# Performance work log

Hardware: AMD Instinct MI355X
Metric: run time of the kernel (lower is better)

Reference implementation:

```python
import jax, jax.numpy as jnp
import numpy as np

THRESHOLD = 0.05
STRIDE = (1, 1)
PADDING = ((1, 1), (1, 1))


def ternary_quantize(w, threshold=THRESHOLD):
    # w -> {-1, 0, +1}; zero where |w| <= threshold
    mask = (jnp.abs(w) > threshold).astype(w.dtype)
    return jnp.sign(w) * mask


def setup_inputs() -> dict:
    key = jax.random.key(0)
    k1, k2 = jax.random.split(key)
    B, Cin, H, W = 32, 256, 56, 56
    Cout, kH, kW = 256, 3, 3
    fan_in = Cin * kH * kW
    std = np.sqrt(2.0 / fan_in) * 2.0
    x = jax.random.normal(k1, (B, Cin, H, W), dtype=jnp.float32)
    weight = jax.random.normal(k2, (Cout, Cin, kH, kW), dtype=jnp.float32) * std
    bias = jnp.zeros((Cout,), dtype=jnp.float32)
    return {"x": x, "weight": weight, "bias": bias}


def reference(x, weight, bias):
    w_t = ternary_quantize(weight, THRESHOLD)
    out = jax.lax.conv_general_dilated(
        x, w_t,
        window_strides=STRIDE,
        padding=PADDING,
        dimension_numbers=("NCHW", "OIHW", "NCHW"),
    )
    return out + bias[None, :, None, None]
```

## Files before the change

### kernel.cpp

```cpp
#include <hip/hip_runtime.h>

#define CIN   256
#define COUT  256
#define HH    56
#define WW    56
#define BATCH 32
#define KTOT  2304
#define HP    58
#define WP    58
#define NPIX  (BATCH*HH*WW)
#define HWSZ  (HH*WW)
#define BN    224
#define NBLK  (NPIX/BN)

typedef __bf16 bf16x8 __attribute__((ext_vector_type(8)));
typedef float  f32x4  __attribute__((ext_vector_type(4)));

#define AS1 __attribute__((address_space(1)))
#define AS3 __attribute__((address_space(3)))

__device__ __forceinline__ unsigned short f2bf(float f) {
  union { float f; unsigned int u; } v; v.f = f;
  unsigned int u = v.u;
  u += 0x7fffu + ((u >> 16) & 1u);
  return (unsigned short)(u >> 16);
}

__device__ __forceinline__ void async16(const void* g, void* l) {
  __builtin_amdgcn_global_load_lds((const AS1 unsigned int*)g,
                                   (AS3 unsigned int*)l, 16, 0, 0);
}

#define TSTR 60
#define QBLKS 2304
__global__ __launch_bounds__(256) void prep(const float* __restrict__ w,
                                            unsigned short* __restrict__ wr,
                                            const float* __restrict__ x,
                                            unsigned short* __restrict__ xp) {
  const int bx = blockIdx.x;
  if (bx < QBLKS) {
    int tid = bx * 256 + threadIdx.x;
    int co  = tid / KTOT;
    int rem = tid - co * KTOT;
    int tap = rem >> 8;
    int ci  = rem & 255;
    int kh  = tap / 3;
    int kw  = tap - kh * 3;
    float v = w[((co * CIN + ci) * 3 + kh) * 3 + kw];
    float q = (fabsf(v) > 0.05f) ? ((v > 0.f) ? 1.f : -1.f) : 0.f;
    wr[tid] = f2bf(q);
    return;
  }
  const int pbx = bx - QBLKS;
  const int nhp = pbx >> 2;
  const int n   = nhp / HP;
  const int hp  = nhp - n * HP;
  const int ci0 = (pbx & 3) << 6;
  const int t   = threadIdx.x;
  const size_t obase = (size_t)nhp * (WP * 256);

  __shared__ __align__(16) float tile[64 * TSTR];
  const bool hborder = (hp == 0) || (hp == HP - 1);

  if (!hborder) {
    const int h = hp - 1;
    #pragma unroll
    for (int it = 0; it < 4; ++it) {
      int linear = it * 256 + t;
      if (linear < 896) {
        int cil = linear / 14;
        int w4  = linear - cil * 14;
        *(float4*)&tile[cil * TSTR + w4 * 4] =
            *(const float4*)&x[(((size_t)(n * CIN + ci0 + cil)) * HH + h) * WW + w4 * 4];
      }
    }
  }
  __syncthreads();

  #pragma unroll
  for (int it = 0; it < 2; ++it) {
    int linear = it * 256 + t;
    if (linear < 464) {
      int wp = linear >> 3;
      int g  = linear & 7;
      unsigned int pk[4] = {0u, 0u, 0u, 0u};
      if (!hborder && wp != 0 && wp != WP - 1) {
        #pragma unroll
        for (int j = 0; j < 4; ++j) {
          int jr = (j + g) & 3;
          unsigned int lo = f2bf(tile[(g * 8 + 2 * jr) * TSTR + (wp - 1)]);
          unsigned int hi = f2bf(tile[(g * 8 + 2 * jr + 1) * TSTR + (wp - 1)]);
          pk[jr] = lo | (hi << 16);
        }
      }
      uint4 v; v.x = pk[0]; v.y = pk[1]; v.z = pk[2]; v.w = pk[3];
      *(uint4*)(xp + obase + (size_t)wp * 256 + ci0 + g * 8) = v;
    }
  }
}


#define NOWAIT (void)0
#define VM4 asm volatile("s_waitcnt vmcnt(4)" ::: "memory")
#define VM0 asm volatile("s_waitcnt vmcnt(0)" ::: "memory")

#define STAGE4(buf_, kn_) do {                                                \
  const int kn__ = (kn_);                                                     \
  const size_t koW_ = (size_t)kn__ << 5;                                      \
  const int tap_ = kn__ >> 3;                                                 \
  const int kh_  = tap_ / 3;                                                  \
  const int kw_  = tap_ - kh_ * 3;                                            \
  const size_t koX_ = (size_t)((kh_ * WP + kw_) * 256 + ((kn__ & 7) << 5));   \
  char* da_ = smem + (buf_) * 32768 + t * 16;                                 \
  char* db_ = smem + (buf_) * 32768 + 16384 + t * 16;                         \
  async16(Wr + koW_ + aSrc0, da_);                                            \
  async16(Wr + koW_ + aSrc1, da_ + 8192);                                     \
  async16(Xp + koX_ + bSrc0, db_);                                            \
  async16(Xp + koX_ + bSrc1, db_ + 8192);                                     \
} while (0)

#define PHASE(buf_, WAITE, ...) do {                                          \
  __VA_ARGS__;                                                                \
  bf16x8 af_[4], bf_[7];                                                      \
  _Pragma("unroll")                                                           \
  for (int mt = 0; mt < 4; ++mt)                                              \
    af_[mt] = *(const bf16x8*)(smem + (buf_) * 32768 + rdA + mt * 1024);      \
  _Pragma("unroll")                                                           \
  for (int nt = 0; nt < 7; ++nt)                                              \
    bf_[nt] = *(const bf16x8*)(smem + (buf_) * 32768 + 16384 + rdB + nt * 1024);\
  _Pragma("unroll")                                                           \
  for (int mt = 0; mt < 4; ++mt)                                              \
    _Pragma("unroll")                                                         \
    for (int nt = 0; nt < 7; ++nt)                                            \
      acc[mt][nt] = __builtin_amdgcn_mfma_f32_16x16x32_bf16(                  \
          af_[mt], bf_[nt], acc[mt][nt], 0, 0, 0);                            \
  WAITE;                                                                      \
  __builtin_amdgcn_s_barrier();                                               \
  __builtin_amdgcn_sched_barrier(0);                                          \
} while (0)

__global__ __launch_bounds__(512, 2) void conv_gemm(
    const unsigned short* __restrict__ Wr,
    const unsigned short* __restrict__ Xp,
    const float* __restrict__ bias,
    float* __restrict__ out) {
  extern __shared__ char smem[];

  const int t    = threadIdx.x;
  const int lane = t & 63;
  const int wv   = t >> 6;
  const int wm   = wv >> 1;
  const int wn   = wv & 1;
  const int l15  = lane & 15;
  const int quad = lane >> 4;

  const int bid = blockIdx.x;
  const int pb  = (bid & 7) * 56 + (bid >> 3);
  const int p0  = pb * BN;

  const int srow = t >> 2;
  const int schk = (t & 3) ^ ((srow >> 1) & 3);

  const size_t aSrc0 = (size_t)srow * KTOT + schk * 8;
  const size_t aSrc1 = aSrc0 + (size_t)128 * KTOT;

  const int pA = p0 + srow;
  const int pB = pA + 128;
  const int nA = pA / HWSZ;  const int hwA = pA - nA * HWSZ;
  const int hA = hwA / WW;   const int wA  = hwA - hA * WW;
  const int nB = pB / HWSZ;  const int hwB = pB - nB * HWSZ;
  const int hB = hwB / WW;   const int wB  = hwB - hB * WW;
  const size_t bSrc0 = ((size_t)((nA * HP + hA) * WP + wA)) * 256 + schk * 8;
  const size_t bSrc1 = ((size_t)((nB * HP + hB) * WP + wB)) * 256 + schk * 8;

  const int rchk = (quad ^ ((l15 >> 1) & 3)) * 16;
  const int rdA  = (wm * 64  + l15) * 64 + rchk;
  const int rdB  = (wn * 112 + l15) * 64 + rchk;

  f32x4 acc[4][7];
  #pragma unroll
  for (int i = 0; i < 4; ++i)
    #pragma unroll
    for (int j = 0; j < 7; ++j)
      acc[i][j] = (f32x4){0.f, 0.f, 0.f, 0.f};

  STAGE4(0, 0);
  STAGE4(1, 1);
  VM4;
  __builtin_amdgcn_s_barrier();
  __builtin_amdgcn_sched_barrier(0);

  #pragma unroll 1
  for (int it = 0; it < 23; ++it) {
    const int k0 = 3 * it;
    PHASE(0, VM4, STAGE4(2, k0 + 2));
    PHASE(1, VM4, STAGE4(0, k0 + 3));
    PHASE(2, VM4, STAGE4(1, k0 + 4));
  }
  PHASE(0, VM4, STAGE4(2, 71));
  PHASE(1, VM0, NOWAIT);
  PHASE(2, NOWAIT, NOWAIT);

  float bv[4][4];
  #pragma unroll
  for (int mt = 0; mt < 4; ++mt)
    #pragma unroll
    for (int r = 0; r < 4; ++r)
      bv[mt][r] = bias[wm * 64 + mt * 16 + quad * 4 + r];

  #pragma unroll
  for (int nt = 0; nt < 7; ++nt) {
    const int p  = p0 + wn * 112 + nt * 16 + l15;
    const int np = p / HWSZ;
    const int hw = p - np * HWSZ;
    const size_t obase = (size_t)np * (COUT * HWSZ) + hw;
    #pragma unroll
    for (int mt = 0; mt < 4; ++mt) {
      const int co = wm * 64 + mt * 16 + quad * 4;
      #pragma unroll
      for (int r = 0; r < 4; ++r)
        out[obase + (size_t)(co + r) * HWSZ] = acc[mt][nt][r] + bv[mt][r];
    }
  }
}

extern "C" void kernel_launch(void* const* d_in, const int* in_sizes, int n_in,
                              void* d_out, int out_size, void* d_ws, size_t ws_size,
                              hipStream_t stream) {
  const float* x    = (const float*)d_in[0];
  const float* w    = (const float*)d_in[1];
  const float* bias = (const float*)d_in[2];
  float* out        = (float*)d_out;

  unsigned short* xp = (unsigned short*)d_ws;
  unsigned short* wr = (unsigned short*)((char*)d_ws + 55115776);

  prep<<<dim3(QBLKS + BATCH * HP * 4), dim3(256), 0, stream>>>(w, wr, x, xp);

  (void)hipFuncSetAttribute((const void*)conv_gemm,
                            hipFuncAttributeMaxDynamicSharedMemorySize, 98304);
  conv_gemm<<<dim3(NBLK), dim3(512), 98304, stream>>>(wr, xp, bias, out);
}
```

Measured before the change: 308.0 us.

## Deepen LDS pipeline to four stages and double-buffer B fragments in registers

```diff
diff --git a/kernel.cpp b/kernel.cpp
--- a/kernel.cpp
+++ b/kernel.cpp
@@ -119,21 +119,23 @@
   async16(Xp + koX_ + bSrc1, db_ + 8192);                                     \
 } while (0)
 
-#define PHASE(buf_, WAITE, ...) do {                                          \
+#define PHASE(bc_, bn_, cur_, nxt_, DOBF_, WAITE, ...) do {                   \
   __VA_ARGS__;                                                                \
-  bf16x8 af_[4], bf_[7];                                                      \
+  bf16x8 af_[4];                                                              \
   _Pragma("unroll")                                                           \
   for (int mt = 0; mt < 4; ++mt)                                              \
-    af_[mt] = *(const bf16x8*)(smem + (buf_) * 32768 + rdA + mt * 1024);      \
-  _Pragma("unroll")                                                           \
-  for (int nt = 0; nt < 7; ++nt)                                              \
-    bf_[nt] = *(const bf16x8*)(smem + (buf_) * 32768 + 16384 + rdB + nt * 1024);\
+    af_[mt] = *(const bf16x8*)(smem + (bc_) * 32768 + rdA + mt * 1024);       \
+  if (DOBF_) {                                                                \
+    _Pragma("unroll")                                                         \
+    for (int nt = 0; nt < 7; ++nt)                                            \
+      nxt_[nt] = *(const bf16x8*)(smem + (bn_) * 32768 + 16384 + rdB + nt * 1024);\
+  }                                                                           \
   _Pragma("unroll")                                                           \
   for (int mt = 0; mt < 4; ++mt)                                              \
     _Pragma("unroll")                                                         \
     for (int nt = 0; nt < 7; ++nt)                                            \
       acc[mt][nt] = __builtin_amdgcn_mfma_f32_16x16x32_bf16(                  \
-          af_[mt], bf_[nt], acc[mt][nt], 0, 0, 0);                            \
+          af_[mt], cur_[nt], acc[mt][nt], 0, 0, 0);                           \
   WAITE;                                                                      \
   __builtin_amdgcn_s_barrier();                                               \
   __builtin_amdgcn_sched_barrier(0);                                          \
@@ -184,22 +186,30 @@
     for (int j = 0; j < 7; ++j)
       acc[i][j] = (f32x4){0.f, 0.f, 0.f, 0.f};
 
+  bf16x8 bfA[7], bfB[7];
+
   STAGE4(0, 0);
   STAGE4(1, 1);
+  STAGE4(2, 2);
   VM4;
   __builtin_amdgcn_s_barrier();
   __builtin_amdgcn_sched_barrier(0);
+  #pragma unroll
+  for (int nt = 0; nt < 7; ++nt)
+    bfA[nt] = *(const bf16x8*)(smem + 16384 + rdB + nt * 1024);
 
   #pragma unroll 1
-  for (int it = 0; it < 23; ++it) {
-    const int k0 = 3 * it;
-    PHASE(0, VM4, STAGE4(2, k0 + 2));
-    PHASE(1, VM4, STAGE4(0, k0 + 3));
-    PHASE(2, VM4, STAGE4(1, k0 + 4));
-  }
-  PHASE(0, VM4, STAGE4(2, 71));
-  PHASE(1, VM0, NOWAIT);
-  PHASE(2, NOWAIT, NOWAIT);
+  for (int it = 0; it < 17; ++it) {
+    const int k0 = 4 * it;
+    PHASE(0, 1, bfA, bfB, 1, VM4, STAGE4(3, k0 + 3));
+    PHASE(1, 2, bfB, bfA, 1, VM4, STAGE4(0, k0 + 4));
+    PHASE(2, 3, bfA, bfB, 1, VM4, STAGE4(1, k0 + 5));
+    PHASE(3, 0, bfB, bfA, 1, VM4, STAGE4(2, k0 + 6));
+  }
+  PHASE(0, 1, bfA, bfB, 1, VM4, STAGE4(3, 71));
+  PHASE(1, 2, bfB, bfA, 1, VM0, NOWAIT);
+  PHASE(2, 3, bfA, bfB, 1, NOWAIT, NOWAIT);
+  PHASE(3, 0, bfB, bfA, 0, NOWAIT, NOWAIT);
 
   float bv[4][4];
   #pragma unroll
@@ -238,6 +248,6 @@
   prep<<<dim3(QBLKS + BATCH * HP * 4), dim3(256), 0, stream>>>(w, wr, x, xp);
 
   (void)hipFuncSetAttribute((const void*)conv_gemm,
-                            hipFuncAttributeMaxDynamicSharedMemorySize, 98304);
-  conv_gemm<<<dim3(NBLK), dim3(512), 98304, stream>>>(wr, xp, bias, out);
-}
+                            hipFuncAttributeMaxDynamicSharedMemorySize, 131072);
+  conv_gemm<<<dim3(NBLK), dim3(512), 131072, stream>>>(wr, xp, bias, out);
+}
```

Measured after the change: 307.5 us. Within noise of the previous version (-0.1%).

## Switch conv GEMM to K=64 double-buffered stages with 8-chunk swizzle and setprio

Applied to the files above, without the earlier changes.

```diff
diff --git a/kernel.cpp b/kernel.cpp
--- a/kernel.cpp
+++ b/kernel.cpp
@@ -101,39 +101,58 @@
 
 
 #define NOWAIT (void)0
-#define VM4 asm volatile("s_waitcnt vmcnt(4)" ::: "memory")
 #define VM0 asm volatile("s_waitcnt vmcnt(0)" ::: "memory")
 
-#define STAGE4(buf_, kn_) do {                                                \
+#define STAGE8(buf_, kn_) do {                                                \
   const int kn__ = (kn_);                                                     \
-  const size_t koW_ = (size_t)kn__ << 5;                                      \
-  const int tap_ = kn__ >> 3;                                                 \
+  const size_t koW_ = (size_t)kn__ << 6;                                      \
+  const int tap_ = kn__ >> 2;                                                 \
   const int kh_  = tap_ / 3;                                                  \
   const int kw_  = tap_ - kh_ * 3;                                            \
-  const size_t koX_ = (size_t)((kh_ * WP + kw_) * 256 + ((kn__ & 7) << 5));   \
+  const size_t koX_ = (size_t)((kh_ * WP + kw_) * 256 + ((kn__ & 3) << 6));   \
   char* da_ = smem + (buf_) * 32768 + t * 16;                                 \
-  char* db_ = smem + (buf_) * 32768 + 16384 + t * 16;                         \
+  char* db_ = smem + 65536 + (buf_) * 32768 + t * 16;                         \
   async16(Wr + koW_ + aSrc0, da_);                                            \
   async16(Wr + koW_ + aSrc1, da_ + 8192);                                     \
-  async16(Xp + koX_ + bSrc0, db_);                                            \
-  async16(Xp + koX_ + bSrc1, db_ + 8192);                                     \
+  async16(Wr + koW_ + aSrc2, da_ + 16384);                                    \
+  async16(Wr + koW_ + aSrc3, da_ + 24576);                                    \
+  async16(Xp + koX_ + bSrc[0], db_);                                          \
+  async16(Xp + koX_ + bSrc[1], db_ + 8192);                                   \
+  async16(Xp + koX_ + bSrc[2], db_ + 16384);                                  \
+  async16(Xp + koX_ + bSrc[3], db_ + 24576);                                  \
 } while (0)
 
-#define PHASE(buf_, WAITE, ...) do {                                          \
+#define PHASE(b_, WAITE, ...) do {                                            \
   __VA_ARGS__;                                                                \
-  bf16x8 af_[4], bf_[7];                                                      \
-  _Pragma("unroll")                                                           \
-  for (int mt = 0; mt < 4; ++mt)                                              \
-    af_[mt] = *(const bf16x8*)(smem + (buf_) * 32768 + rdA + mt * 1024);      \
+  const int ab_ = (b_) * 32768;                                               \
+  const int bb_ = 65536 + (b_) * 32768;                                       \
+  bf16x8 af0_[4], bf0_[7], af1_[4], bf1_[7];                                  \
+  _Pragma("unroll")                                                           \
+  for (int mt = 0; mt < 4; ++mt)                                              \
+    af0_[mt] = *(const bf16x8*)(smem + ab_ + rdA + mt * 2048 + cX0);          \
   _Pragma("unroll")                                                           \
   for (int nt = 0; nt < 7; ++nt)                                              \
-    bf_[nt] = *(const bf16x8*)(smem + (buf_) * 32768 + 16384 + rdB + nt * 1024);\
+    bf0_[nt] = *(const bf16x8*)(smem + bb_ + rdB + nt * 2048 + cX0);          \
+  _Pragma("unroll")                                                           \
+  for (int mt = 0; mt < 4; ++mt)                                              \
+    af1_[mt] = *(const bf16x8*)(smem + ab_ + rdA + mt * 2048 + cX1);          \
+  _Pragma("unroll")                                                           \
+  for (int nt = 0; nt < 7; ++nt)                                              \
+    bf1_[nt] = *(const bf16x8*)(smem + bb_ + rdB + nt * 2048 + cX1);          \
+  __builtin_amdgcn_s_setprio(1);                                              \
   _Pragma("unroll")                                                           \
   for (int mt = 0; mt < 4; ++mt)                                              \
     _Pragma("unroll")                                                         \
     for (int nt = 0; nt < 7; ++nt)                                            \
       acc[mt][nt] = __builtin_amdgcn_mfma_f32_16x16x32_bf16(                  \
-          af_[mt], bf_[nt], acc[mt][nt], 0, 0, 0);                            \
+          af0_[mt], bf0_[nt], acc[mt][nt], 0, 0, 0);                          \
+  _Pragma("unroll")                                                           \
+  for (int mt = 0; mt < 4; ++mt)                                              \
+    _Pragma("unroll")                                                         \
+    for (int nt = 0; nt < 7; ++nt)                                            \
+      acc[mt][nt] = __builtin_amdgcn_mfma_f32_16x16x32_bf16(                  \
+          af1_[mt], bf1_[nt], acc[mt][nt], 0, 0, 0);                          \
+  __builtin_amdgcn_s_setprio(0);                                              \
   WAITE;                                                                      \
   __builtin_amdgcn_s_barrier();                                               \
   __builtin_amdgcn_sched_barrier(0);                                          \
@@ -158,24 +177,27 @@
   const int pb  = (bid & 7) * 56 + (bid >> 3);
   const int p0  = pb * BN;
 
-  const int srow = t >> 2;
-  const int schk = (t & 3) ^ ((srow >> 1) & 3);
-
-  const size_t aSrc0 = (size_t)srow * KTOT + schk * 8;
-  const size_t aSrc1 = aSrc0 + (size_t)128 * KTOT;
-
-  const int pA = p0 + srow;
-  const int pB = pA + 128;
-  const int nA = pA / HWSZ;  const int hwA = pA - nA * HWSZ;
-  const int hA = hwA / WW;   const int wA  = hwA - hA * WW;
-  const int nB = pB / HWSZ;  const int hwB = pB - nB * HWSZ;
-  const int hB = hwB / WW;   const int wB  = hwB - hB * WW;
-  const size_t bSrc0 = ((size_t)((nA * HP + hA) * WP + wA)) * 256 + schk * 8;
-  const size_t bSrc1 = ((size_t)((nB * HP + hB) * WP + wB)) * 256 + schk * 8;
-
-  const int rchk = (quad ^ ((l15 >> 1) & 3)) * 16;
-  const int rdA  = (wm * 64  + l15) * 64 + rchk;
-  const int rdB  = (wn * 112 + l15) * 64 + rchk;
+  const int srow  = t >> 3;
+  const int sclog = (t & 7) ^ (srow & 7);
+
+  const size_t aSrc0 = (size_t)srow * KTOT + sclog * 8;
+  const size_t aSrc1 = aSrc0 + (size_t)64  * KTOT;
+  const size_t aSrc2 = aSrc0 + (size_t)128 * KTOT;
+  const size_t aSrc3 = aSrc0 + (size_t)192 * KTOT;
+
+  size_t bSrc[4];
+  #pragma unroll
+  for (int s = 0; s < 4; ++s) {
+    int p = p0 + s * 64 + srow;
+    int n = p / HWSZ; int hw = p - n * HWSZ;
+    int h = hw / WW;  int w = hw - h * WW;
+    bSrc[s] = ((size_t)((n * HP + h) * WP + w)) * 256 + sclog * 8;
+  }
+
+  const int rdA = (wm * 64  + l15) * 128;
+  const int rdB = (wn * 112 + l15) * 128;
+  const int cX0 = ((quad     ^ (lane & 7)) * 16);
+  const int cX1 = (((4+quad) ^ (lane & 7)) * 16);
 
   f32x4 acc[4][7];
   #pragma unroll
@@ -184,22 +206,18 @@
     for (int j = 0; j < 7; ++j)
       acc[i][j] = (f32x4){0.f, 0.f, 0.f, 0.f};
 
-  STAGE4(0, 0);
-  STAGE4(1, 1);
-  VM4;
+  STAGE8(0, 0);
+  VM0;
   __builtin_amdgcn_s_barrier();
   __builtin_amdgcn_sched_barrier(0);
 
   #pragma unroll 1
-  for (int it = 0; it < 23; ++it) {
-    const int k0 = 3 * it;
-    PHASE(0, VM4, STAGE4(2, k0 + 2));
-    PHASE(1, VM4, STAGE4(0, k0 + 3));
-    PHASE(2, VM4, STAGE4(1, k0 + 4));
-  }
-  PHASE(0, VM4, STAGE4(2, 71));
-  PHASE(1, VM0, NOWAIT);
-  PHASE(2, NOWAIT, NOWAIT);
+  for (int it = 0; it < 17; ++it) {
+    PHASE(0, VM0, STAGE8(1, 2 * it + 1));
+    PHASE(1, VM0, STAGE8(0, 2 * it + 2));
+  }
+  PHASE(0, VM0, STAGE8(1, 35));
+  PHASE(1, NOWAIT, NOWAIT);
 
   float bv[4][4];
   #pragma unroll
@@ -238,6 +256,6 @@
   prep<<<dim3(QBLKS + BATCH * HP * 4), dim3(256), 0, stream>>>(w, wr, x, xp);
 
   (void)hipFuncSetAttribute((const void*)conv_gemm,
-                            hipFuncAttributeMaxDynamicSharedMemorySize, 98304);
-  conv_gemm<<<dim3(NBLK), dim3(512), 98304, stream>>>(wr, xp, bias, out);
-}
+                            hipFuncAttributeMaxDynamicSharedMemorySize, 131072);
+  conv_gemm<<<dim3(NBLK), dim3(512), 131072, stream>>>(wr, xp, bias, out);
+}
```

Result: no change. 313.5 us (+1.8%).
